# Performance work log

Hardware: AMD Instinct MI355X
Metric: run time of the kernel (lower is better)

Reference implementation:

```python
import jax, jax.numpy as jnp
import numpy as np
from jax import lax

V, E, C_OUT, K, NTAGS = 32000, 256, 256, 3, 32
B, T = 64, 2048


def setup_inputs() -> dict:
    key = jax.random.key(0)
    ks = jax.random.split(key, 12)
    inputs = jax.random.randint(ks[0], (B, T), 0, V)
    emb_table = jax.random.normal(ks[1], (V, E), jnp.float32) * 0.02
    emb_table = emb_table.at[1].set(0.0)  # padding_idx=1
    conv1_w = jax.random.normal(ks[2], (C_OUT, E, K), jnp.float32) * 0.02
    conv1_b = jax.random.normal(ks[3], (C_OUT,), jnp.float32) * 0.02
    conv2_w = jax.random.normal(ks[4], (C_OUT, C_OUT, K), jnp.float32) * 0.02
    conv2_b = jax.random.normal(ks[5], (C_OUT,), jnp.float32) * 0.02
    fc_w = jax.random.normal(ks[6], (NTAGS, E), jnp.float32) * 0.02
    fc_b = jax.random.normal(ks[7], (NTAGS,), jnp.float32) * 0.02
    trans = jax.random.normal(ks[8], (NTAGS, NTAGS), jnp.float32) * 0.1
    start_t = jax.random.normal(ks[9], (NTAGS,), jnp.float32) * 0.1
    end_t = jax.random.normal(ks[10], (NTAGS,), jnp.float32) * 0.1
    return {"inputs": inputs, "emb_table": emb_table,
            "conv1_w": conv1_w, "conv1_b": conv1_b,
            "conv2_w": conv2_w, "conv2_b": conv2_b,
            "fc_w": fc_w, "fc_b": fc_b,
            "trans": trans, "start_t": start_t, "end_t": end_t}


def _conv1d(x, w, b):
    # x: [B, C_in, T], w: [C_out, C_in, K], padding=1
    y = lax.conv_general_dilated(x, w, window_strides=(1,), padding=[(1, 1)],
                                 dimension_numbers=("NCH", "OIH", "NCH"))
    return y + b[None, :, None]


def _crf_log_partition(emissions, trans, start_t, end_t):
    # emissions: [B, T, NTAGS] -> logZ per sequence [B]
    em_t = jnp.swapaxes(emissions, 0, 1)  # [T, B, NTAGS]
    alpha0 = start_t[None, :] + em_t[0]   # [B, NTAGS]

    def step(alpha, emit):
        # alpha: [B, C]; broadcast prev-tag x next-tag: [B, C, C]
        scores = alpha[:, :, None] + trans[None, :, :] + emit[:, None, :]
        new_alpha = jax.scipy.special.logsumexp(scores, axis=1)
        return new_alpha, None

    alpha, _ = lax.scan(step, alpha0, em_t[1:])
    return jax.scipy.special.logsumexp(alpha + end_t[None, :], axis=-1)


def reference(inputs, emb_table, conv1_w, conv1_b, conv2_w, conv2_b,
              fc_w, fc_b, trans, start_t, end_t):
    emb = emb_table[inputs]                    # [B, T, E]
    x = jnp.swapaxes(emb, 1, 2)                # [B, E, T]
    x = _conv1d(x, conv1_w, conv1_b)           # [B, C, T]
    x = _conv1d(x, conv2_w, conv2_b)           # [B, C, T]
    h = jnp.swapaxes(x, 1, 2)                  # [B, T, E]  (dropout = identity in eval)
    logits = jnp.einsum("bte,ce->btc", h, fc_w) + fc_b  # [B, T, NTAGS]
    return _crf_log_partition(logits, trans, start_t, end_t)  # [B]
```

## Files before the change

kernel.cpp:

```cpp
#include <hip/hip_runtime.h>
#include <hip/hip_bf16.h>

typedef float f32x4 __attribute__((ext_vector_type(4)));
typedef __bf16 bf16x8 __attribute__((ext_vector_type(8)));
typedef __bf16 bf16x4 __attribute__((ext_vector_type(4)));

__global__ __launch_bounds__(256) void transpose_w(const float* __restrict__ w1,
                                                   const float* __restrict__ w2,
                                                   float* __restrict__ w1t,
                                                   float* __restrict__ w2t) {
  int tid = blockIdx.x * 256 + threadIdx.x;
  if (tid < 196608) {
    float v = w1[tid];
    int k1 = tid % 3;
    int r = tid / 3;
    int e = r & 255;
    int cp = r >> 8;
    w1t[(k1 * 256 + e) * 256 + cp] = v;
  } else {
    int t2 = tid - 196608;
    float v = w2[t2];
    int k2 = t2 % 3;
    int r = t2 / 3;
    int cp = r & 255;
    int c = r >> 8;
    w2t[(k2 * 256 + cp) * 256 + c] = v;
  }
}

__global__ __launch_bounds__(256) void prep_g(const float* __restrict__ fcw,
                                              const float* __restrict__ w2t,
                                              float* __restrict__ G) {
  int tid = blockIdx.x * 256 + threadIdx.x;
  int cp = tid & 255;
  int rest = tid >> 8;
  int n = rest & 31;
  int k2 = rest >> 5;
  const float* wr = w2t + (k2 * 256 + cp) * 256;
  const float* fr = fcw + n * 256;
  float acc = 0.f;
  #pragma unroll 8
  for (int c = 0; c < 256; c += 4) {
    f32x4 a = *(const f32x4*)(fr + c);
    f32x4 bb = *(const f32x4*)(wr + c);
    acc = fmaf(a[0], bb[0], acc); acc = fmaf(a[1], bb[1], acc);
    acc = fmaf(a[2], bb[2], acc); acc = fmaf(a[3], bb[3], acc);
  }
  G[(k2 * 32 + n) * 256 + cp] = acc;
}

__global__ __launch_bounds__(256) void prep_wf(const float* __restrict__ G,
                                               const float* __restrict__ w1t,
                                               const float* __restrict__ b1,
                                               const float* __restrict__ b2,
                                               const float* __restrict__ fcw,
                                               const float* __restrict__ fcb,
                                               __bf16* __restrict__ wfb,
                                               float* __restrict__ C0,
                                               float* __restrict__ CT,
                                               float* __restrict__ bias_tot,
                                               float* __restrict__ c0v,
                                               float* __restrict__ cTv) {
  int tid = blockIdx.x * 256 + threadIdx.x;
  if (tid < 40960) {
    int n = tid & 31;
    int r = tid >> 5;
    int kk = r % 5;
    int e = r / 5;
    float acc = 0.f;
    #pragma unroll
    for (int k2 = 0; k2 < 3; ++k2) {
      int k1 = kk - k2;
      if (k1 < 0 || k1 > 2) continue;
      const float* g = G + (k2 * 32 + n) * 256;
      const float* wr = w1t + (k1 * 256 + e) * 256;
      #pragma unroll 8
      for (int cp = 0; cp < 256; cp += 4) {
        f32x4 a = *(const f32x4*)(g + cp);
        f32x4 bb = *(const f32x4*)(wr + cp);
        acc = fmaf(a[0], bb[0], acc); acc = fmaf(a[1], bb[1], acc);
        acc = fmaf(a[2], bb[2], acc); acc = fmaf(a[3], bb[3], acc);
      }
    }
    int j = kk * 32 + n;
    int jt = j >> 4, jl = j & 15;
    int et = e >> 5, el = e & 31;
    int lane = jl | ((el >> 3) << 4);
    int rr = el & 7;
    wfb[((jt * 8 + et) * 64 + lane) * 8 + rr] = (__bf16)acc;
  } else if (tid < 57344) {
    int t2 = tid - 40960;
    int which = (t2 >= 8192);
    if (which) t2 -= 8192;
    int n = t2 & 31;
    int e = t2 >> 5;
    const float* g = G + ((which ? 2 : 0) * 32 + n) * 256;
    int k1 = which ? 0 : 2;
    const float* wr = w1t + (k1 * 256 + e) * 256;
    float acc = 0.f;
    #pragma unroll 8
    for (int cp = 0; cp < 256; cp += 4) {
      f32x4 a = *(const f32x4*)(g + cp);
      f32x4 bb = *(const f32x4*)(wr + cp);
      acc = fmaf(a[0], bb[0], acc); acc = fmaf(a[1], bb[1], acc);
      acc = fmaf(a[2], bb[2], acc); acc = fmaf(a[3], bb[3], acc);
    }
    (which ? CT : C0)[n * 256 + e] = acc;
  } else if (tid < 57376) {
    int n = tid - 57344;
    float bt = fcb[n];
    for (int c = 0; c < 256; ++c) bt = fmaf(fcw[n * 256 + c], b2[c], bt);
    float s0 = 0.f, s1 = 0.f, s2 = 0.f;
    const float* g0 = G + (0 * 32 + n) * 256;
    const float* g1 = G + (1 * 32 + n) * 256;
    const float* g2 = G + (2 * 32 + n) * 256;
    for (int cp = 0; cp < 256; ++cp) {
      s0 = fmaf(g0[cp], b1[cp], s0);
      s1 = fmaf(g1[cp], b1[cp], s1);
      s2 = fmaf(g2[cp], b1[cp], s2);
    }
    bias_tot[n] = bt + s0 + s1 + s2;
    c0v[n] = s0;
    cTv[n] = s2;
  }
}

__global__ __launch_bounds__(256) void corr_k(const int* __restrict__ idx,
                                              const float* __restrict__ emb,
                                              const float* __restrict__ C0,
                                              const float* __restrict__ CT,
                                              const float* __restrict__ c0v,
                                              const float* __restrict__ cTv,
                                              float* __restrict__ corr) {
  __shared__ float red[256];
  int b = blockIdx.x >> 1;
  int which = blockIdx.x & 1;
  int n = threadIdx.x & 31;
  int part = threadIdx.x >> 5;
  int v = idx[b * 2048 + (which ? 2047 : 0)];
  const float* C = which ? CT : C0;
  const float* er = emb + v * 256 + part * 32;
  const float* cr = C + n * 256 + part * 32;
  float s = 0.f;
  #pragma unroll
  for (int e = 0; e < 32; ++e) s = fmaf(cr[e], er[e], s);
  red[threadIdx.x] = s;
  __syncthreads();
  if (part == 0) {
    float tot = (which ? cTv : c0v)[n];
    #pragma unroll
    for (int p = 0; p < 8; ++p) tot += red[p * 32 + n];
    corr[(which * 64 + b) * 32 + n] = tot;
  }
}

__global__ __launch_bounds__(256) void p_table(const float* __restrict__ emb,
                                               const __bf16* __restrict__ wfb,
                                               __bf16* __restrict__ P) {
  int lane = threadIdx.x & 63;
  int mt = blockIdx.x * 4 + (threadIdx.x >> 6);
  int ln = lane & 15;
  int q = lane >> 4;
  int m = mt * 16 + ln;
  f32x4 acc[10];
  #pragma unroll
  for (int jt = 0; jt < 10; ++jt) acc[jt] = (f32x4){0.f, 0.f, 0.f, 0.f};
  const float* arow = emb + m * 256 + q * 8;
  #pragma unroll
  for (int et = 0; et < 8; ++et) {
    f32x4 a0 = *(const f32x4*)(arow + et * 32);
    f32x4 a1 = *(const f32x4*)(arow + et * 32 + 4);
    bf16x8 af;
    af[0] = (__bf16)a0[0]; af[1] = (__bf16)a0[1];
    af[2] = (__bf16)a0[2]; af[3] = (__bf16)a0[3];
    af[4] = (__bf16)a1[0]; af[5] = (__bf16)a1[1];
    af[6] = (__bf16)a1[2]; af[7] = (__bf16)a1[3];
    #pragma unroll
    for (int jt = 0; jt < 10; ++jt) {
      bf16x8 bfr = *(const bf16x8*)(wfb + ((jt * 8 + et) * 64 + lane) * 8);
      acc[jt] = __builtin_amdgcn_mfma_f32_16x16x32_bf16(af, bfr, acc[jt], 0, 0, 0);
    }
  }
  #pragma unroll
  for (int jt = 0; jt < 10; ++jt) {
    __bf16* pp = P + (mt * 16 + q * 4) * 160 + jt * 16 + ln;
    pp[0]   = (__bf16)acc[jt][0];
    pp[160] = (__bf16)acc[jt][1];
    pp[320] = (__bf16)acc[jt][2];
    pp[480] = (__bf16)acc[jt][3];
  }
}

__global__ __launch_bounds__(256) void logits_k(const int* __restrict__ idx,
                                                const __bf16* __restrict__ P,
                                                const float* __restrict__ bias_tot,
                                                const float* __restrict__ corr,
                                                float* __restrict__ L) {
  int tid = blockIdx.x * 256 + threadIdx.x;
  int q = tid & 7;
  int tp = (tid >> 3) & 1023;
  int b = tid >> 13;
  int t0 = tp * 2;
  const int* ib = idx + b * 2048;
  f32x4 bias = *(const f32x4*)(bias_tot + q * 4);
  f32x4 acc0 = bias, acc1 = bias;
  #pragma unroll
  for (int j = 0; j < 6; ++j) {
    int tt = t0 + j - 2;
    if (tt < 0 || tt > 2047) continue;
    int v = ib[tt];
    const __bf16* pr = P + v * 160 + q * 4;
    if (j < 5) {
      bf16x4 pv = *(const bf16x4*)(pr + j * 32);
      acc0[0] += (float)pv[0]; acc0[1] += (float)pv[1];
      acc0[2] += (float)pv[2]; acc0[3] += (float)pv[3];
    }
    if (j >= 1) {
      bf16x4 pv = *(const bf16x4*)(pr + (j - 1) * 32);
      acc1[0] += (float)pv[0]; acc1[1] += (float)pv[1];
      acc1[2] += (float)pv[2]; acc1[3] += (float)pv[3];
    }
  }
  if (t0 == 0)        acc0 -= *(const f32x4*)(corr + b * 32 + q * 4);
  if (t0 + 1 == 2047) acc1 -= *(const f32x4*)(corr + (64 + b) * 32 + q * 4);
  f32x4 r0, r1;
  r0[0] = __expf(acc0[0]) * 0.03125f;
  r0[1] = __expf(acc0[1]) * 0.03125f;
  r0[2] = __expf(acc0[2]) * 0.03125f;
  r0[3] = __expf(acc0[3]) * 0.03125f;
  r1[0] = __expf(acc1[0]) * 0.03125f;
  r1[1] = __expf(acc1[1]) * 0.03125f;
  r1[2] = __expf(acc1[2]) * 0.03125f;
  r1[3] = __expf(acc1[3]) * 0.03125f;
  float* Lb = L + (b * 2048 + t0) * 32 + q * 4;
  *(f32x4*)(Lb) = r0;
  *(f32x4*)(Lb + 32) = r1;
}

__global__ __launch_bounds__(256) void crf_stage1(const float* __restrict__ Lexp,
                                                  const float* __restrict__ trans,
                                                  float* __restrict__ Pc) {
  __shared__ __bf16 sl[4][32 * 40];
  int lane = threadIdx.x & 63;
  int w = threadIdx.x >> 6;
  int chain = blockIdx.x * 4 + w;
  int c = chain >> 6;
  int b = chain & 63;
  int ln = lane & 15;
  int q = lane >> 4;
  float tA0[8], tA1[8];
  #pragma unroll
  for (int e = 0; e < 8; ++e) {
    tA0[e] = __expf(trans[(q * 8 + e) * 32 + ln]);
    tA1[e] = __expf(trans[(q * 8 + e) * 32 + 16 + ln]);
  }
  bf16x8 bf0, bf1;
  #pragma unroll
  for (int e = 0; e < 8; ++e) {
    int k = q * 8 + e;
    bf0[e] = (k == ln) ? (__bf16)1.0f : (__bf16)0.0f;
    bf1[e] = (k == 16 + ln) ? (__bf16)1.0f : (__bf16)0.0f;
  }
  int tstart = c * 32 + 1;
  int nsteps = (c == 63) ? 31 : 32;
  const float* Le = Lexp + (b * 2048 + tstart) * 32;
  __bf16* myS = &sl[w][0];
  f32x4 c00, c01, c10, c11;
  float sc0 = Le[ln], sc1 = Le[ln + 16];
  for (int s = 0; s < nsteps; ++s) {
    float nsc0 = 0.f, nsc1 = 0.f;
    if (s + 1 < nsteps) {
      nsc0 = Le[(s + 1) * 32 + ln];
      nsc1 = Le[(s + 1) * 32 + ln + 16];
    }
    bf16x8 a0, a1;
    #pragma unroll
    for (int e = 0; e < 8; ++e) {
      a0[e] = (__bf16)(sc0 * tA0[e]);
      a1[e] = (__bf16)(sc1 * tA1[e]);
    }
    f32x4 z = {0.f, 0.f, 0.f, 0.f};
    c00 = __builtin_amdgcn_mfma_f32_16x16x32_bf16(a0, bf0, z, 0, 0, 0);
    c01 = __builtin_amdgcn_mfma_f32_16x16x32_bf16(a0, bf1, z, 0, 0, 0);
    c10 = __builtin_amdgcn_mfma_f32_16x16x32_bf16(a1, bf0, z, 0, 0, 0);
    c11 = __builtin_amdgcn_mfma_f32_16x16x32_bf16(a1, bf1, z, 0, 0, 0);
    if (s + 1 < nsteps) {
      bf16x4 w00, w01, w10, w11;
      #pragma unroll
      for (int r = 0; r < 4; ++r) {
        w00[r] = (__bf16)c00[r]; w01[r] = (__bf16)c01[r];
        w10[r] = (__bf16)c10[r]; w11[r] = (__bf16)c11[r];
      }
      *(bf16x4*)(myS + (ln) * 40      + q * 4)      = w00;
      *(bf16x4*)(myS + (16 + ln) * 40 + q * 4)      = w01;
      *(bf16x4*)(myS + (ln) * 40      + 16 + q * 4) = w10;
      *(bf16x4*)(myS + (16 + ln) * 40 + 16 + q * 4) = w11;
      bf0 = *(const bf16x8*)(myS + (ln) * 40 + q * 8);
      bf1 = *(const bf16x8*)(myS + (16 + ln) * 40 + q * 8);
    }
    sc0 = nsc0; sc1 = nsc1;
  }
  float* dst = Pc + ((b * 64 + c) * 32) * 32;
  *(f32x4*)(dst + (ln) * 32      + q * 4)      = c00;
  *(f32x4*)(dst + (16 + ln) * 32 + q * 4)      = c01;
  *(f32x4*)(dst + (ln) * 32      + 16 + q * 4) = c10;
  *(f32x4*)(dst + (16 + ln) * 32 + 16 + q * 4) = c11;
}

__global__ __launch_bounds__(256) void crf_comb8(const float* __restrict__ Pc,
                                                 float* __restrict__ Pg) {
  __shared__ __bf16 sl[4][32 * 40];
  int lane = threadIdx.x & 63;
  int w = threadIdx.x >> 6;
  int wave = blockIdx.x * 4 + w;
  int b = wave >> 3;
  int g = wave & 7;
  int ln = lane & 15;
  int q = lane >> 4;
  const float* base = Pc + ((b * 64 + g * 8) * 32) * 32;
  float cur[16], nxt[16];
  #pragma unroll
  for (int e = 0; e < 8; ++e) {
    cur[e]     = base[(q * 8 + e) * 32 + ln];
    cur[8 + e] = base[(q * 8 + e) * 32 + 16 + ln];
  }
  bf16x8 bf0, bf1;
  #pragma unroll
  for (int e = 0; e < 8; ++e) {
    int k = q * 8 + e;
    bf0[e] = (k == ln) ? (__bf16)1.0f : (__bf16)0.0f;
    bf1[e] = (k == 16 + ln) ? (__bf16)1.0f : (__bf16)0.0f;
  }
  __bf16* myS = &sl[w][0];
  f32x4 c00, c01, c10, c11;
  for (int j = 0; j < 8; ++j) {
    if (j < 7) {
      const float* mn = base + (j + 1) * 1024;
      #pragma unroll
      for (int e = 0; e < 8; ++e) {
        nxt[e]     = mn[(q * 8 + e) * 32 + ln];
        nxt[8 + e] = mn[(q * 8 + e) * 32 + 16 + ln];
      }
    }
    bf16x8 a0, a1;
    #pragma unroll
    for (int e = 0; e < 8; ++e) {
      a0[e] = (__bf16)cur[e];
      a1[e] = (__bf16)cur[8 + e];
    }
    f32x4 z = {0.f, 0.f, 0.f, 0.f};
    c00 = __builtin_amdgcn_mfma_f32_16x16x32_bf16(a0, bf0, z, 0, 0, 0);
    c01 = __builtin_amdgcn_mfma_f32_16x16x32_bf16(a0, bf1, z, 0, 0, 0);
    c10 = __builtin_amdgcn_mfma_f32_16x16x32_bf16(a1, bf0, z, 0, 0, 0);
    c11 = __builtin_amdgcn_mfma_f32_16x16x32_bf16(a1, bf1, z, 0, 0, 0);
    if (j < 7) {
      bf16x4 w00, w01, w10, w11;
      #pragma unroll
      for (int r = 0; r < 4; ++r) {
        w00[r] = (__bf16)c00[r]; w01[r] = (__bf16)c01[r];
        w10[r] = (__bf16)c10[r]; w11[r] = (__bf16)c11[r];
      }
      *(bf16x4*)(myS + (ln) * 40      + q * 4)      = w00;
      *(bf16x4*)(myS + (16 + ln) * 40 + q * 4)      = w01;
      *(bf16x4*)(myS + (ln) * 40      + 16 + q * 4) = w10;
      *(bf16x4*)(myS + (16 + ln) * 40 + 16 + q * 4) = w11;
      bf0 = *(const bf16x8*)(myS + (ln) * 40 + q * 8);
      bf1 = *(const bf16x8*)(myS + (16 + ln) * 40 + q * 8);
      #pragma unroll
      for (int e = 0; e < 16; ++e) cur[e] = nxt[e];
    }
  }
  float* dst = Pg + ((b * 8 + g) * 32) * 32;
  *(f32x4*)(dst + (ln) * 32      + q * 4)      = c00;
  *(f32x4*)(dst + (16 + ln) * 32 + q * 4)      = c01;
  *(f32x4*)(dst + (ln) * 32      + 16 + q * 4) = c10;
  *(f32x4*)(dst + (16 + ln) * 32 + 16 + q * 4) = c11;
}

__global__ __launch_bounds__(256) void crf_final(const float* __restrict__ Lexp,
                                                 const float* __restrict__ Pg,
                                                 const float* __restrict__ start_t,
                                                 const float* __restrict__ end_t,
                                                 float* __restrict__ out) {
  __shared__ float sm[8192];
  int b = blockIdx.x;
  int tid = threadIdx.x;
  int j = tid & 31;
  const float* base = Pg + b * 8192;
  #pragma unroll
  for (int g = 0; g < 8; ++g)
    *(f32x4*)(&sm[g * 1024 + tid * 4]) = *(const f32x4*)(base + g * 1024 + tid * 4);
  float u = __expf(start_t[j]) * Lexp[b * 2048 * 32 + j] * 32.f;
  __syncthreads();
  float logacc = 0.f;
  #pragma unroll
  for (int g = 0; g < 8; ++g) {
    const float* M = &sm[g * 1024];
    float nu0 = 0.f, nu1 = 0.f, nu2 = 0.f, nu3 = 0.f;
    #pragma unroll
    for (int k = 0; k < 32; k += 4) {
      nu0 = fmaf(__shfl(u, k,     32), M[(k)     * 32 + j], nu0);
      nu1 = fmaf(__shfl(u, k + 1, 32), M[(k + 1) * 32 + j], nu1);
      nu2 = fmaf(__shfl(u, k + 2, 32), M[(k + 2) * 32 + j], nu2);
      nu3 = fmaf(__shfl(u, k + 3, 32), M[(k + 3) * 32 + j], nu3);
    }
    float nu = (nu0 + nu1) + (nu2 + nu3);
    float ssum = nu;
    #pragma unroll
    for (int o = 1; o < 32; o <<= 1) ssum += __shfl_xor(ssum, o, 32);
    u = nu * __builtin_amdgcn_rcpf(ssum);
    logacc += __logf(ssum);
  }
  float term = u * __expf(end_t[j]);
  #pragma unroll
  for (int o = 1; o < 32; o <<= 1) term += __shfl_xor(term, o, 32);
  if (tid == 0)
    out[b] = logacc + logf(term) + (float)(2047.0 * 5.0 * 0.69314718055994530942);
}

extern "C" void kernel_launch(void* const* d_in, const int* in_sizes, int n_in,
                              void* d_out, int out_size, void* d_ws, size_t ws_size,
                              hipStream_t stream) {
  const int*   idx  = (const int*)d_in[0];
  const float* emb  = (const float*)d_in[1];
  const float* w1   = (const float*)d_in[2];
  const float* b1   = (const float*)d_in[3];
  const float* w2   = (const float*)d_in[4];
  const float* b2   = (const float*)d_in[5];
  const float* fcw  = (const float*)d_in[6];
  const float* fcb  = (const float*)d_in[7];
  const float* trn  = (const float*)d_in[8];
  const float* st   = (const float*)d_in[9];
  const float* en   = (const float*)d_in[10];

  char* ws = (char*)d_ws;
  __bf16* P     = (__bf16*)(ws + 0);
  float*  Pg    = (float*)(ws + 0);
  float*  L     = (float*)(ws + 10240000);
  float*  Pc    = (float*)(ws + 27017216);
  float*  w1t   = (float*)(ws + 27017216);
  float*  w2t   = (float*)(ws + 27803648);
  __bf16* WfB   = (__bf16*)(ws + 43794432);
  float*  G     = (float*)(ws + 43876352);
  float*  C0    = (float*)(ws + 43974656);
  float*  CT    = (float*)(ws + 44007424);
  float*  bias  = (float*)(ws + 44040192);
  float*  c0v   = (float*)(ws + 44040320);
  float*  cTv   = (float*)(ws + 44040448);
  float*  corr  = (float*)(ws + 44040576);

  transpose_w<<<1536, 256, 0, stream>>>(w1, w2, w1t, w2t);
  prep_g     <<<96,   256, 0, stream>>>(fcw, w2t, G);
  prep_wf    <<<225,  256, 0, stream>>>(G, w1t, b1, b2, fcw, fcb, WfB, C0, CT, bias, c0v, cTv);
  corr_k     <<<128,  256, 0, stream>>>(idx, emb, C0, CT, c0v, cTv, corr);
  p_table    <<<500,  256, 0, stream>>>(emb, WfB, P);
  logits_k   <<<2048, 256, 0, stream>>>(idx, P, bias, corr, L);
  crf_stage1 <<<1024, 256, 0, stream>>>(L, trn, Pc);
  crf_comb8  <<<128,  256, 0, stream>>>(Pc, Pg);
  crf_final  <<<64,   256, 0, stream>>>(L, Pg, st, en, (float*)d_out);
}
```

Baseline: 193.6 us.

## Fuse kernels, store CRF emissions and partial products in bf16, batch loads

Merges the correction kernel into the P-table kernel and the CRF combine and final kernels into one tail kernel, removing two launches. Exponentiated emissions and the per-chunk transfer matrices are now stored in bf16 instead of fp32, halving that memory traffic. The stage-1 chain prefetches emissions eight steps at a time to hide load latency. The chain is now seeded from bf16-rounded emissions, which costs some precision.

Result: faster. 186.6 us (-3.6%).

```diff
diff --git a/kernel.cpp b/kernel.cpp
--- a/kernel.cpp
+++ b/kernel.cpp
@@ -125,69 +125,70 @@
   }
 }
 
-__global__ __launch_bounds__(256) void corr_k(const int* __restrict__ idx,
-                                              const float* __restrict__ emb,
-                                              const float* __restrict__ C0,
-                                              const float* __restrict__ CT,
-                                              const float* __restrict__ c0v,
-                                              const float* __restrict__ cTv,
-                                              float* __restrict__ corr) {
+__global__ __launch_bounds__(256) void ptab_corr(const float* __restrict__ emb,
+                                                 const __bf16* __restrict__ wfb,
+                                                 __bf16* __restrict__ P,
+                                                 const int* __restrict__ idx,
+                                                 const float* __restrict__ C0,
+                                                 const float* __restrict__ CT,
+                                                 const float* __restrict__ c0v,
+                                                 const float* __restrict__ cTv,
+                                                 float* __restrict__ corr) {
   __shared__ float red[256];
-  int b = blockIdx.x >> 1;
-  int which = blockIdx.x & 1;
-  int n = threadIdx.x & 31;
-  int part = threadIdx.x >> 5;
-  int v = idx[b * 2048 + (which ? 2047 : 0)];
-  const float* C = which ? CT : C0;
-  const float* er = emb + v * 256 + part * 32;
-  const float* cr = C + n * 256 + part * 32;
-  float s = 0.f;
-  #pragma unroll
-  for (int e = 0; e < 32; ++e) s = fmaf(cr[e], er[e], s);
-  red[threadIdx.x] = s;
-  __syncthreads();
-  if (part == 0) {
-    float tot = (which ? cTv : c0v)[n];
-    #pragma unroll
-    for (int p = 0; p < 8; ++p) tot += red[p * 32 + n];
-    corr[(which * 64 + b) * 32 + n] = tot;
-  }
-}
-
-__global__ __launch_bounds__(256) void p_table(const float* __restrict__ emb,
-                                               const __bf16* __restrict__ wfb,
-                                               __bf16* __restrict__ P) {
-  int lane = threadIdx.x & 63;
-  int mt = blockIdx.x * 4 + (threadIdx.x >> 6);
-  int ln = lane & 15;
-  int q = lane >> 4;
-  int m = mt * 16 + ln;
-  f32x4 acc[10];
-  #pragma unroll
-  for (int jt = 0; jt < 10; ++jt) acc[jt] = (f32x4){0.f, 0.f, 0.f, 0.f};
-  const float* arow = emb + m * 256 + q * 8;
-  #pragma unroll
-  for (int et = 0; et < 8; ++et) {
-    f32x4 a0 = *(const f32x4*)(arow + et * 32);
-    f32x4 a1 = *(const f32x4*)(arow + et * 32 + 4);
-    bf16x8 af;
-    af[0] = (__bf16)a0[0]; af[1] = (__bf16)a0[1];
-    af[2] = (__bf16)a0[2]; af[3] = (__bf16)a0[3];
-    af[4] = (__bf16)a1[0]; af[5] = (__bf16)a1[1];
-    af[6] = (__bf16)a1[2]; af[7] = (__bf16)a1[3];
+  if (blockIdx.x < 500) {
+    int lane = threadIdx.x & 63;
+    int mt = blockIdx.x * 4 + (threadIdx.x >> 6);
+    int ln = lane & 15;
+    int q = lane >> 4;
+    int m = mt * 16 + ln;
+    f32x4 acc[10];
+    #pragma unroll
+    for (int jt = 0; jt < 10; ++jt) acc[jt] = (f32x4){0.f, 0.f, 0.f, 0.f};
+    const float* arow = emb + m * 256 + q * 8;
+    #pragma unroll
+    for (int et = 0; et < 8; ++et) {
+      f32x4 a0 = *(const f32x4*)(arow + et * 32);
+      f32x4 a1 = *(const f32x4*)(arow + et * 32 + 4);
+      bf16x8 af;
+      af[0] = (__bf16)a0[0]; af[1] = (__bf16)a0[1];
+      af[2] = (__bf16)a0[2]; af[3] = (__bf16)a0[3];
+      af[4] = (__bf16)a1[0]; af[5] = (__bf16)a1[1];
+      af[6] = (__bf16)a1[2]; af[7] = (__bf16)a1[3];
+      #pragma unroll
+      for (int jt = 0; jt < 10; ++jt) {
+        bf16x8 bfr = *(const bf16x8*)(wfb + ((jt * 8 + et) * 64 + lane) * 8);
+        acc[jt] = __builtin_amdgcn_mfma_f32_16x16x32_bf16(af, bfr, acc[jt], 0, 0, 0);
+      }
+    }
     #pragma unroll
     for (int jt = 0; jt < 10; ++jt) {
-      bf16x8 bfr = *(const bf16x8*)(wfb + ((jt * 8 + et) * 64 + lane) * 8);
-      acc[jt] = __builtin_amdgcn_mfma_f32_16x16x32_bf16(af, bfr, acc[jt], 0, 0, 0);
-    }
-  }
-  #pragma unroll
-  for (int jt = 0; jt < 10; ++jt) {
-    __bf16* pp = P + (mt * 16 + q * 4) * 160 + jt * 16 + ln;
-    pp[0]   = (__bf16)acc[jt][0];
-    pp[160] = (__bf16)acc[jt][1];
-    pp[320] = (__bf16)acc[jt][2];
-    pp[480] = (__bf16)acc[jt][3];
+      __bf16* pp = P + (mt * 16 + q * 4) * 160 + jt * 16 + ln;
+      pp[0]   = (__bf16)acc[jt][0];
+      pp[160] = (__bf16)acc[jt][1];
+      pp[320] = (__bf16)acc[jt][2];
+      pp[480] = (__bf16)acc[jt][3];
+    }
+  } else {
+    int bid = blockIdx.x - 500;
+    int b = bid >> 1;
+    int which = bid & 1;
+    int n = threadIdx.x & 31;
+    int part = threadIdx.x >> 5;
+    int v = idx[b * 2048 + (which ? 2047 : 0)];
+    const float* C = which ? CT : C0;
+    const float* er = emb + v * 256 + part * 32;
+    const float* cr = C + n * 256 + part * 32;
+    float s = 0.f;
+    #pragma unroll
+    for (int e = 0; e < 32; ++e) s = fmaf(cr[e], er[e], s);
+    red[threadIdx.x] = s;
+    __syncthreads();
+    if (part == 0) {
+      float tot = (which ? cTv : c0v)[n];
+      #pragma unroll
+      for (int p = 0; p < 8; ++p) tot += red[p * 32 + n];
+      corr[(which * 64 + b) * 32 + n] = tot;
+    }
   }
 }
 
@@ -195,7 +196,7 @@
                                                 const __bf16* __restrict__ P,
                                                 const float* __restrict__ bias_tot,
                                                 const float* __restrict__ corr,
-                                                float* __restrict__ L) {
+                                                __bf16* __restrict__ L) {
   int tid = blockIdx.x * 256 + threadIdx.x;
   int q = tid & 7;
   int tp = (tid >> 3) & 1023;
@@ -223,23 +224,23 @@
   }
   if (t0 == 0)        acc0 -= *(const f32x4*)(corr + b * 32 + q * 4);
   if (t0 + 1 == 2047) acc1 -= *(const f32x4*)(corr + (64 + b) * 32 + q * 4);
-  f32x4 r0, r1;
-  r0[0] = __expf(acc0[0]) * 0.03125f;
-  r0[1] = __expf(acc0[1]) * 0.03125f;
-  r0[2] = __expf(acc0[2]) * 0.03125f;
-  r0[3] = __expf(acc0[3]) * 0.03125f;
-  r1[0] = __expf(acc1[0]) * 0.03125f;
-  r1[1] = __expf(acc1[1]) * 0.03125f;
-  r1[2] = __expf(acc1[2]) * 0.03125f;
-  r1[3] = __expf(acc1[3]) * 0.03125f;
-  float* Lb = L + (b * 2048 + t0) * 32 + q * 4;
-  *(f32x4*)(Lb) = r0;
-  *(f32x4*)(Lb + 32) = r1;
-}
-
-__global__ __launch_bounds__(256) void crf_stage1(const float* __restrict__ Lexp,
+  bf16x4 r0, r1;
+  r0[0] = (__bf16)(__expf(acc0[0]) * 0.03125f);
+  r0[1] = (__bf16)(__expf(acc0[1]) * 0.03125f);
+  r0[2] = (__bf16)(__expf(acc0[2]) * 0.03125f);
+  r0[3] = (__bf16)(__expf(acc0[3]) * 0.03125f);
+  r1[0] = (__bf16)(__expf(acc1[0]) * 0.03125f);
+  r1[1] = (__bf16)(__expf(acc1[1]) * 0.03125f);
+  r1[2] = (__bf16)(__expf(acc1[2]) * 0.03125f);
+  r1[3] = (__bf16)(__expf(acc1[3]) * 0.03125f);
+  __bf16* Lb = L + (b * 2048 + t0) * 32 + q * 4;
+  *(bf16x4*)(Lb) = r0;
+  *(bf16x4*)(Lb + 32) = r1;
+}
+
+__global__ __launch_bounds__(256) void crf_stage1(const __bf16* __restrict__ Lexp,
                                                   const float* __restrict__ trans,
-                                                  float* __restrict__ Pc) {
+                                                  __bf16* __restrict__ PcB) {
   __shared__ __bf16 sl[4][32 * 40];
   int lane = threadIdx.x & 63;
   int w = threadIdx.x >> 6;
@@ -262,17 +263,11 @@
     bf1[e] = (k == 16 + ln) ? (__bf16)1.0f : (__bf16)0.0f;
   }
   int tstart = c * 32 + 1;
-  int nsteps = (c == 63) ? 31 : 32;
-  const float* Le = Lexp + (b * 2048 + tstart) * 32;
+  int total = (c == 63) ? 31 : 32;
+  const __bf16* Le = Lexp + (b * 2048 + tstart) * 32;
   __bf16* myS = &sl[w][0];
-  f32x4 c00, c01, c10, c11;
-  float sc0 = Le[ln], sc1 = Le[ln + 16];
-  for (int s = 0; s < nsteps; ++s) {
-    float nsc0 = 0.f, nsc1 = 0.f;
-    if (s + 1 < nsteps) {
-      nsc0 = Le[(s + 1) * 32 + ln];
-      nsc1 = Le[(s + 1) * 32 + ln + 16];
-    }
+
+  auto step = [&](float sc0, float sc1) {
     bf16x8 a0, a1;
     #pragma unroll
     for (int e = 0; e < 8; ++e) {
@@ -280,50 +275,80 @@
       a1[e] = (__bf16)(sc1 * tA1[e]);
     }
     f32x4 z = {0.f, 0.f, 0.f, 0.f};
-    c00 = __builtin_amdgcn_mfma_f32_16x16x32_bf16(a0, bf0, z, 0, 0, 0);
-    c01 = __builtin_amdgcn_mfma_f32_16x16x32_bf16(a0, bf1, z, 0, 0, 0);
-    c10 = __builtin_amdgcn_mfma_f32_16x16x32_bf16(a1, bf0, z, 0, 0, 0);
-    c11 = __builtin_amdgcn_mfma_f32_16x16x32_bf16(a1, bf1, z, 0, 0, 0);
-    if (s + 1 < nsteps) {
-      bf16x4 w00, w01, w10, w11;
+    f32x4 c00 = __builtin_amdgcn_mfma_f32_16x16x32_bf16(a0, bf0, z, 0, 0, 0);
+    f32x4 c01 = __builtin_amdgcn_mfma_f32_16x16x32_bf16(a0, bf1, z, 0, 0, 0);
+    f32x4 c10 = __builtin_amdgcn_mfma_f32_16x16x32_bf16(a1, bf0, z, 0, 0, 0);
+    f32x4 c11 = __builtin_amdgcn_mfma_f32_16x16x32_bf16(a1, bf1, z, 0, 0, 0);
+    bf16x4 w00, w01, w10, w11;
+    #pragma unroll
+    for (int r = 0; r < 4; ++r) {
+      w00[r] = (__bf16)c00[r]; w01[r] = (__bf16)c01[r];
+      w10[r] = (__bf16)c10[r]; w11[r] = (__bf16)c11[r];
+    }
+    *(bf16x4*)(myS + (ln) * 40      + q * 4)      = w00;
+    *(bf16x4*)(myS + (16 + ln) * 40 + q * 4)      = w01;
+    *(bf16x4*)(myS + (ln) * 40      + 16 + q * 4) = w10;
+    *(bf16x4*)(myS + (16 + ln) * 40 + 16 + q * 4) = w11;
+    bf0 = *(const bf16x8*)(myS + (ln) * 40 + q * 8);
+    bf1 = *(const bf16x8*)(myS + (16 + ln) * 40 + q * 8);
+  };
+
+  float s0[8], s1[8];
+  #pragma unroll
+  for (int i = 0; i < 8; ++i) {
+    s0[i] = (float)Le[i * 32 + ln];
+    s1[i] = (float)Le[i * 32 + 16 + ln];
+  }
+  int nbatch = total >> 3;
+  int rem = total & 7;
+  for (int bt = 0; bt < nbatch; ++bt) {
+    float n0[8], n1[8];
+    bool more = (bt + 1 < nbatch) || (rem != 0 && bt + 1 == nbatch);
+    if (more) {
+      int bs = (bt + 1) * 8;
       #pragma unroll
-      for (int r = 0; r < 4; ++r) {
-        w00[r] = (__bf16)c00[r]; w01[r] = (__bf16)c01[r];
-        w10[r] = (__bf16)c10[r]; w11[r] = (__bf16)c11[r];
+      for (int i = 0; i < 8; ++i) {
+        int k = bs + i; if (k >= total) k = total - 1;
+        n0[i] = (float)Le[k * 32 + ln];
+        n1[i] = (float)Le[k * 32 + 16 + ln];
       }
-      *(bf16x4*)(myS + (ln) * 40      + q * 4)      = w00;
-      *(bf16x4*)(myS + (16 + ln) * 40 + q * 4)      = w01;
-      *(bf16x4*)(myS + (ln) * 40      + 16 + q * 4) = w10;
-      *(bf16x4*)(myS + (16 + ln) * 40 + 16 + q * 4) = w11;
-      bf0 = *(const bf16x8*)(myS + (ln) * 40 + q * 8);
-      bf1 = *(const bf16x8*)(myS + (16 + ln) * 40 + q * 8);
-    }
-    sc0 = nsc0; sc1 = nsc1;
-  }
-  float* dst = Pc + ((b * 64 + c) * 32) * 32;
-  *(f32x4*)(dst + (ln) * 32      + q * 4)      = c00;
-  *(f32x4*)(dst + (16 + ln) * 32 + q * 4)      = c01;
-  *(f32x4*)(dst + (ln) * 32      + 16 + q * 4) = c10;
-  *(f32x4*)(dst + (16 + ln) * 32 + 16 + q * 4) = c11;
-}
-
-__global__ __launch_bounds__(256) void crf_comb8(const float* __restrict__ Pc,
-                                                 float* __restrict__ Pg) {
-  __shared__ __bf16 sl[4][32 * 40];
-  int lane = threadIdx.x & 63;
-  int w = threadIdx.x >> 6;
-  int wave = blockIdx.x * 4 + w;
-  int b = wave >> 3;
-  int g = wave & 7;
+    }
+    #pragma unroll
+    for (int s = 0; s < 8; ++s) step(s0[s], s1[s]);
+    #pragma unroll
+    for (int i = 0; i < 8; ++i) { s0[i] = n0[i]; s1[i] = n1[i]; }
+  }
+  if (rem) {
+    #pragma unroll
+    for (int s = 0; s < 7; ++s) step(s0[s], s1[s]);
+  }
+  bf16x8 o0, o1;
+  #pragma unroll
+  for (int e = 0; e < 8; ++e) {
+    o0[e] = myS[(q * 8 + e) * 40 + ln];
+    o1[e] = myS[(q * 8 + e) * 40 + 16 + ln];
+  }
+  __bf16* dst = PcB + ((b * 64 + c) * 64 + lane) * 16;
+  *(bf16x8*)(dst)     = o0;
+  *(bf16x8*)(dst + 8) = o1;
+}
+
+__global__ __launch_bounds__(512) void crf_tail(const __bf16* __restrict__ Lexp,
+                                                const __bf16* __restrict__ PcB,
+                                                const float* __restrict__ start_t,
+                                                const float* __restrict__ end_t,
+                                                float* __restrict__ out) {
+  __shared__ float sg[8][1024];
+  __shared__ __bf16 sl[8][32 * 40];
+  int b = blockIdx.x;
+  int tid = threadIdx.x;
+  int lane = tid & 63;
+  int g = tid >> 6;
   int ln = lane & 15;
   int q = lane >> 4;
-  const float* base = Pc + ((b * 64 + g * 8) * 32) * 32;
-  float cur[16], nxt[16];
-  #pragma unroll
-  for (int e = 0; e < 8; ++e) {
-    cur[e]     = base[(q * 8 + e) * 32 + ln];
-    cur[8 + e] = base[(q * 8 + e) * 32 + 16 + ln];
-  }
+  const __bf16* base = PcB + ((b * 64 + g * 8) * 64) * 16;
+  bf16x8 a0 = *(const bf16x8*)(base + lane * 16);
+  bf16x8 a1 = *(const bf16x8*)(base + lane * 16 + 8);
   bf16x8 bf0, bf1;
   #pragma unroll
   for (int e = 0; e < 8; ++e) {
@@ -331,22 +356,14 @@
     bf0[e] = (k == ln) ? (__bf16)1.0f : (__bf16)0.0f;
     bf1[e] = (k == 16 + ln) ? (__bf16)1.0f : (__bf16)0.0f;
   }
-  __bf16* myS = &sl[w][0];
+  __bf16* myS = &sl[g][0];
   f32x4 c00, c01, c10, c11;
   for (int j = 0; j < 8; ++j) {
+    bf16x8 na0, na1;
     if (j < 7) {
-      const float* mn = base + (j + 1) * 1024;
-      #pragma unroll
-      for (int e = 0; e < 8; ++e) {
-        nxt[e]     = mn[(q * 8 + e) * 32 + ln];
-        nxt[8 + e] = mn[(q * 8 + e) * 32 + 16 + ln];
-      }
-    }
-    bf16x8 a0, a1;
-    #pragma unroll
-    for (int e = 0; e < 8; ++e) {
-      a0[e] = (__bf16)cur[e];
-      a1[e] = (__bf16)cur[8 + e];
+      const __bf16* nb = base + (j + 1) * 1024 + lane * 16;
+      na0 = *(const bf16x8*)(nb);
+      na1 = *(const bf16x8*)(nb + 8);
     }
     f32x4 z = {0.f, 0.f, 0.f, 0.f};
     c00 = __builtin_amdgcn_mfma_f32_16x16x32_bf16(a0, bf0, z, 0, 0, 0);
@@ -366,43 +383,30 @@
       *(bf16x4*)(myS + (16 + ln) * 40 + 16 + q * 4) = w11;
       bf0 = *(const bf16x8*)(myS + (ln) * 40 + q * 8);
       bf1 = *(const bf16x8*)(myS + (16 + ln) * 40 + q * 8);
-      #pragma unroll
-      for (int e = 0; e < 16; ++e) cur[e] = nxt[e];
-    }
-  }
-  float* dst = Pg + ((b * 8 + g) * 32) * 32;
-  *(f32x4*)(dst + (ln) * 32      + q * 4)      = c00;
-  *(f32x4*)(dst + (16 + ln) * 32 + q * 4)      = c01;
-  *(f32x4*)(dst + (ln) * 32      + 16 + q * 4) = c10;
-  *(f32x4*)(dst + (16 + ln) * 32 + 16 + q * 4) = c11;
-}
-
-__global__ __launch_bounds__(256) void crf_final(const float* __restrict__ Lexp,
-                                                 const float* __restrict__ Pg,
-                                                 const float* __restrict__ start_t,
-                                                 const float* __restrict__ end_t,
-                                                 float* __restrict__ out) {
-  __shared__ float sm[8192];
-  int b = blockIdx.x;
-  int tid = threadIdx.x;
-  int j = tid & 31;
-  const float* base = Pg + b * 8192;
-  #pragma unroll
-  for (int g = 0; g < 8; ++g)
-    *(f32x4*)(&sm[g * 1024 + tid * 4]) = *(const f32x4*)(base + g * 1024 + tid * 4);
-  float u = __expf(start_t[j]) * Lexp[b * 2048 * 32 + j] * 32.f;
+      a0 = na0; a1 = na1;
+    }
+  }
+  #pragma unroll
+  for (int r = 0; r < 4; ++r) {
+    sg[g][(ln) * 32      + q * 4 + r]      = c00[r];
+    sg[g][(16 + ln) * 32 + q * 4 + r]      = c01[r];
+    sg[g][(ln) * 32      + 16 + q * 4 + r] = c10[r];
+    sg[g][(16 + ln) * 32 + 16 + q * 4 + r] = c11[r];
+  }
+  int j2 = tid & 31;
+  float u = __expf(start_t[j2]) * (float)Lexp[b * 2048 * 32 + j2] * 32.f;
   __syncthreads();
   float logacc = 0.f;
   #pragma unroll
-  for (int g = 0; g < 8; ++g) {
-    const float* M = &sm[g * 1024];
+  for (int gg = 0; gg < 8; ++gg) {
+    const float* M = &sg[gg][0];
     float nu0 = 0.f, nu1 = 0.f, nu2 = 0.f, nu3 = 0.f;
     #pragma unroll
     for (int k = 0; k < 32; k += 4) {
-      nu0 = fmaf(__shfl(u, k,     32), M[(k)     * 32 + j], nu0);
-      nu1 = fmaf(__shfl(u, k + 1, 32), M[(k + 1) * 32 + j], nu1);
-      nu2 = fmaf(__shfl(u, k + 2, 32), M[(k + 2) * 32 + j], nu2);
-      nu3 = fmaf(__shfl(u, k + 3, 32), M[(k + 3) * 32 + j], nu3);
+      nu0 = fmaf(__shfl(u, k,     32), M[(k)     * 32 + j2], nu0);
+      nu1 = fmaf(__shfl(u, k + 1, 32), M[(k + 1) * 32 + j2], nu1);
+      nu2 = fmaf(__shfl(u, k + 2, 32), M[(k + 2) * 32 + j2], nu2);
+      nu3 = fmaf(__shfl(u, k + 3, 32), M[(k + 3) * 32 + j2], nu3);
     }
     float nu = (nu0 + nu1) + (nu2 + nu3);
     float ssum = nu;
@@ -411,7 +415,7 @@
     u = nu * __builtin_amdgcn_rcpf(ssum);
     logacc += __logf(ssum);
   }
-  float term = u * __expf(end_t[j]);
+  float term = u * __expf(end_t[j2]);
   #pragma unroll
   for (int o = 1; o < 32; o <<= 1) term += __shfl_xor(term, o, 32);
   if (tid == 0)
@@ -435,9 +439,8 @@
 
   char* ws = (char*)d_ws;
   __bf16* P     = (__bf16*)(ws + 0);
-  float*  Pg    = (float*)(ws + 0);
-  float*  L     = (float*)(ws + 10240000);
-  float*  Pc    = (float*)(ws + 27017216);
+  __bf16* L     = (__bf16*)(ws + 10240000);
+  __bf16* PcB   = (__bf16*)(ws + 18628608);
   float*  w1t   = (float*)(ws + 27017216);
   float*  w2t   = (float*)(ws + 27803648);
   __bf16* WfB   = (__bf16*)(ws + 43794432);
@@ -452,10 +455,8 @@
   transpose_w<<<1536, 256, 0, stream>>>(w1, w2, w1t, w2t);
   prep_g     <<<96,   256, 0, stream>>>(fcw, w2t, G);
   prep_wf    <<<225,  256, 0, stream>>>(G, w1t, b1, b2, fcw, fcb, WfB, C0, CT, bias, c0v, cTv);
-  corr_k     <<<128,  256, 0, stream>>>(idx, emb, C0, CT, c0v, cTv, corr);
-  p_table    <<<500,  256, 0, stream>>>(emb, WfB, P);
+  ptab_corr  <<<628,  256, 0, stream>>>(emb, WfB, P, idx, C0, CT, c0v, cTv, corr);
   logits_k   <<<2048, 256, 0, stream>>>(idx, P, bias, corr, L);
-  crf_stage1 <<<1024, 256, 0, stream>>>(L, trn, Pc);
-  crf_comb8  <<<128,  256, 0, stream>>>(Pc, Pg);
-  crf_final  <<<64,   256, 0, stream>>>(L, Pg, st, en, (float*)d_out);
-}
+  crf_stage1 <<<1024, 256, 0, stream>>>(L, trn, PcB);
+  crf_tail   <<<64,   512, 0, stream>>>(L, PcB, st, en, (float*)d_out);
+}
```
